# Optimization experiments

Measured on AMD Instinct MI355X. Metric: run time of the kernel, lower is better.

The kernel has to match this reference:

```python
import jax, jax.numpy as jnp
import numpy as np

T, B, D, H = 512, 64, 256, 512


def setup_inputs() -> dict:
    key = jax.random.key(0)
    ks = jax.random.split(key, 6)
    scale = 1.0 / np.sqrt(D + H)
    return {
        "seqs": jax.random.normal(ks[0], (T, B, D), dtype=jnp.float32),
        "h": jnp.zeros((B, H), dtype=jnp.float32),
        "C": jnp.zeros((B, H), dtype=jnp.float32),
        "Wi": jax.random.normal(ks[1], (H, D + H), dtype=jnp.float32) * scale,
        "bi": jnp.zeros((H,), dtype=jnp.float32),
        "Wf": jax.random.normal(ks[2], (H, D + H), dtype=jnp.float32) * scale,
        "bf": jnp.zeros((H,), dtype=jnp.float32),
        "Wg": jax.random.normal(ks[3], (H, D + H), dtype=jnp.float32) * scale,
        "bg": jnp.zeros((H,), dtype=jnp.float32),
        "Wo": jax.random.normal(ks[4], (H, D + H), dtype=jnp.float32) * scale,
        "bo": jnp.zeros((H,), dtype=jnp.float32),
    }


def reference(seqs, h, C, Wi, bi, Wf, bf, Wg, bg, Wo, bo):
    # Fuse the 4 gate Linears into one matmul: W [4H, D+H], b [4H].
    W = jnp.concatenate([Wi, Wf, Wg, Wo], axis=0)
    b = jnp.concatenate([bi, bf, bg, bo], axis=0)

    def step(carry, x):
        h_t, c_t = carry
        merge = jnp.concatenate([h_t, x], axis=1)  # [B, H+D] (h first, as in torch code)
        gates = merge @ W.T + b                    # [B, 4H]
        i, f, g, o = jnp.split(gates, 4, axis=1)
        c_new = jax.nn.sigmoid(f) * c_t + jax.nn.sigmoid(i) * jnp.tanh(g)
        h_new = jax.nn.sigmoid(o) * jnp.tanh(c_new)
        return (h_new, c_new), h_new

    (_, cT), hs = jax.lax.scan(step, (h, C), seqs)
    allhidden = jnp.concatenate([h[None], hs], axis=0)  # [T+1, B, H], includes initial h
    return allhidden, cT
```

## Files before the change

### kernel.cpp

```cpp
#include <hip/hip_runtime.h>


#define TSTEPS 512
#define BATCH 64
#define DIN 256
#define HID 512
#define KTOT 768
#define BHID (BATCH * HID)
#define NB 8
#define NU 16
#define VROW 1064
#define POISON 0x7f7f7f7fu

typedef __attribute__((ext_vector_type(8))) short bf16x8;
typedef __attribute__((ext_vector_type(4))) float f32x4;

__device__ __forceinline__ float4 llc_load4(const float* p) {
    float4 r; asm volatile("global_load_dwordx4 %0, %1, off sc0 sc1" : "=v"(r) : "v"(p)); return r;
}
__device__ __forceinline__ float llc_load1(const float* p) {
    float r; asm volatile("global_load_dword %0, %1, off sc0 sc1" : "=v"(r) : "v"(p)); return r;
}
__device__ __forceinline__ void llc_store1(float* p, float v) {
    asm volatile("global_store_dword %0, %1, off sc0 sc1" :: "v"(p), "v"(v) : "memory");
}
__device__ __forceinline__ unsigned short f2bf(float f) {
    unsigned u = __float_as_uint(f);
    return (unsigned short)((u + 0x7fffu + ((u >> 16) & 1u)) >> 16);
}

__global__ __launch_bounds__(256, 1)
void lstm_persistent(const float* __restrict__ seqs,
                     const float* __restrict__ h0,
                     const float* __restrict__ c0,
                     const float* __restrict__ Wi, const float* __restrict__ bi,
                     const float* __restrict__ Wf, const float* __restrict__ bff,
                     const float* __restrict__ Wg, const float* __restrict__ bg,
                     const float* __restrict__ Wo, const float* __restrict__ bo,
                     float* __restrict__ out)
{
    __shared__ __align__(16) short vv[NB * VROW];
    __shared__ float red[4][16][12];
    __shared__ float c_s[128];
    __shared__ float bias_s[64];

    const int tid  = threadIdx.x;
    const int bid  = blockIdx.x;
    const int g    = bid >> 5;
    const int rblk = bid & 31;
    const int b0 = g * NB;
    const int u0 = rblk * NU;

    const int w   = tid >> 6;
    const int l   = tid & 63;
    const int n16 = l & 15;
    const int khi = (l >> 4) & 3;
    const int bbr = l & 7;

    const float* Wsel = (w == 0) ? Wi : (w == 1) ? Wf : (w == 2) ? Wg : Wo;
    const float* wrow = Wsel + (size_t)(u0 + n16) * KTOT;
    bf16x8 whi[24], wlo[24];
#pragma unroll
    for (int kt = 0; kt < 24; ++kt) {
        const int k0 = kt * 32 + khi * 8;
        const float4 a = *reinterpret_cast<const float4*>(wrow + k0);
        const float4 b = *reinterpret_cast<const float4*>(wrow + k0 + 4);
        const float vals[8] = {a.x, a.y, a.z, a.w, b.x, b.y, b.z, b.w};
        bf16x8 h8, l8;
#pragma unroll
        for (int i = 0; i < 8; ++i) {
            const unsigned short hv = f2bf(vals[i]);
            h8[i] = (short)hv;
            l8[i] = (short)f2bf(vals[i] - __uint_as_float((unsigned)hv << 16));
        }
        whi[kt] = h8; wlo[kt] = l8;
    }

    if (tid < 64) {
        const int gg = tid >> 4, uu = tid & 15;
        const float* bsel = (gg == 0) ? bi : (gg == 1) ? bff : (gg == 2) ? bg : bo;
        bias_s[tid] = bsel[u0 + uu];
    }
    if (tid < 128) {
        const int uu = tid & 15, bb = tid >> 4;
        c_s[tid] = c0[(size_t)(b0 + bb) * HID + u0 + uu];
        out[(size_t)(b0 + bb) * HID + u0 + uu] = h0[(size_t)(b0 + bb) * HID + u0 + uu];
    }

    {
        const int b = tid >> 5, k0 = (tid & 31) * 16;
        const float* hp = h0 + (size_t)(b0 + b) * HID + k0;
        float hv[16];
#pragma unroll
        for (int i = 0; i < 4; ++i) {
            const float4 t4 = reinterpret_cast<const float4*>(hp)[i];
            hv[4*i] = t4.x; hv[4*i+1] = t4.y; hv[4*i+2] = t4.z; hv[4*i+3] = t4.w;
        }
        bf16x8 a8, b8;
#pragma unroll
        for (int i = 0; i < 8; ++i) { a8[i] = (short)f2bf(hv[i]); b8[i] = (short)f2bf(hv[8+i]); }
        *reinterpret_cast<bf16x8*>(&vv[b * VROW + k0])     = a8;
        *reinterpret_cast<bf16x8*>(&vv[b * VROW + k0 + 8]) = b8;
    }
    if (tid < 128) {
        const int b = tid >> 4, kx = (tid & 15) * 16;
        const float* xp = seqs + (size_t)(b0 + b) * DIN + kx;
        float xv[16];
#pragma unroll
        for (int i = 0; i < 4; ++i) {
            const float4 t4 = reinterpret_cast<const float4*>(xp)[i];
            xv[4*i] = t4.x; xv[4*i+1] = t4.y; xv[4*i+2] = t4.z; xv[4*i+3] = t4.w;
        }
        bf16x8 a8, b8, la8, lb8;
#pragma unroll
        for (int i = 0; i < 8; ++i) {
            const unsigned short h1 = f2bf(xv[i]);
            a8[i] = (short)h1; la8[i] = (short)f2bf(xv[i] - __uint_as_float((unsigned)h1 << 16));
            const unsigned short h2 = f2bf(xv[8+i]);
            b8[i] = (short)h2; lb8[i] = (short)f2bf(xv[8+i] - __uint_as_float((unsigned)h2 << 16));
        }
        *reinterpret_cast<bf16x8*>(&vv[b * VROW + 512 + kx])     = a8;
        *reinterpret_cast<bf16x8*>(&vv[b * VROW + 512 + kx + 8]) = b8;
        *reinterpret_cast<bf16x8*>(&vv[b * VROW + 768 + kx])     = la8;
        *reinterpret_cast<bf16x8*>(&vv[b * VROW + 768 + kx + 8]) = lb8;
    }
    __syncthreads();

    const short* vrow = &vv[bbr * VROW + khi * 8];

    for (int t = 0; t < TSTEPS; ++t) {
        f32x4 aA = {0.f,0.f,0.f,0.f}, aB = {0.f,0.f,0.f,0.f}, aC = {0.f,0.f,0.f,0.f};
#pragma unroll
        for (int kt = 0; kt < 8; ++kt) {
            const bf16x8 bh = *reinterpret_cast<const bf16x8*>(vrow + 512 + kt * 32);
            const bf16x8 bl = *reinterpret_cast<const bf16x8*>(vrow + 768 + kt * 32);
            aA = __builtin_amdgcn_mfma_f32_16x16x32_bf16(whi[16 + kt], bh, aA, 0, 0, 0);
            aB = __builtin_amdgcn_mfma_f32_16x16x32_bf16(wlo[16 + kt], bh, aB, 0, 0, 0);
            aC = __builtin_amdgcn_mfma_f32_16x16x32_bf16(whi[16 + kt], bl, aC, 0, 0, 0);
        }

        float4 xr[4];
        const bool do_x = (t + 1 < TSTEPS) && (tid < 128);
        if (do_x) {
            const float* xp = seqs + (size_t)(t + 1) * BATCH * DIN
                            + (size_t)(b0 + (tid >> 4)) * DIN + (tid & 15) * 16;
#pragma unroll
            for (int i = 0; i < 4; ++i) xr[i] = reinterpret_cast<const float4*>(xp)[i];
        }

        if (t > 0) {
            const float* srow = out + (size_t)t * BHID + (size_t)(b0 + 7) * HID;
            unsigned miss = 0;
            for (;;) {
                bool ok = true;
                if (l < 32) {
                    const float s = llc_load1(srow + l * 16 + 15);
                    asm volatile("s_waitcnt vmcnt(0)" ::: "memory");
                    __builtin_amdgcn_sched_barrier(0);
                    ok = (__float_as_uint(s) != POISON);
                }
                if (__all(ok)) break;
                if (++miss > (1u << 20)) break;
                __builtin_amdgcn_s_sleep(1);
            }
            const int b = tid >> 5, k0 = (tid & 31) * 16;
            const float* hp = out + (size_t)t * BHID + (size_t)(b0 + b) * HID + k0;
            float4 hb[4];
#pragma unroll
            for (int i = 0; i < 4; ++i) hb[i] = llc_load4(hp + 4 * i);
            asm volatile("s_waitcnt vmcnt(0)" ::: "memory");
            __builtin_amdgcn_sched_barrier(0);
            float hv[16];
#pragma unroll
            for (int i = 0; i < 4; ++i) {
                hv[4*i] = hb[i].x; hv[4*i+1] = hb[i].y; hv[4*i+2] = hb[i].z; hv[4*i+3] = hb[i].w;
            }
            bf16x8 a8, b8;
#pragma unroll
            for (int i = 0; i < 8; ++i) { a8[i] = (short)f2bf(hv[i]); b8[i] = (short)f2bf(hv[8+i]); }
            *reinterpret_cast<bf16x8*>(&vv[b * VROW + k0])     = a8;
            *reinterpret_cast<bf16x8*>(&vv[b * VROW + k0 + 8]) = b8;
        }
        __syncthreads();

#pragma unroll
        for (int kt = 0; kt < 16; ++kt) {
            const bf16x8 bh = *reinterpret_cast<const bf16x8*>(vrow + kt * 32);
            aA = __builtin_amdgcn_mfma_f32_16x16x32_bf16(whi[kt], bh, aA, 0, 0, 0);
            aB = __builtin_amdgcn_mfma_f32_16x16x32_bf16(wlo[kt], bh, aB, 0, 0, 0);
        }
        const f32x4 gAcc = aA + aB + aC;
        if (n16 < 8) {
#pragma unroll
            for (int r = 0; r < 4; ++r)
                red[w][khi * 4 + r][n16] = gAcc[r];
        }
        __syncthreads();

        float hn127 = 0.f;
        float* op127 = nullptr;
        if (tid < 128) {
            const int uu = tid & 15, bb = tid >> 4;
            const float gi = red[0][uu][bb] + bias_s[uu];
            const float gf = red[1][uu][bb] + bias_s[16 + uu];
            const float gG = red[2][uu][bb] + bias_s[32 + uu];
            const float go = red[3][uu][bb] + bias_s[48 + uu];
            const float i_ = 1.f / (1.f + __expf(-gi));
            const float f_ = 1.f / (1.f + __expf(-gf));
            const float o_ = 1.f / (1.f + __expf(-go));
            float eg = __expf(-2.f * fabsf(gG));
            float tg = (1.f - eg) / (1.f + eg);
            tg = (gG < 0.f) ? -tg : tg;
            const float cn = f_ * c_s[tid] + i_ * tg;
            c_s[tid] = cn;
            float ec = __expf(-2.f * fabsf(cn));
            float tc = (1.f - ec) / (1.f + ec);
            tc = (cn < 0.f) ? -tc : tc;
            const float hn = o_ * tc;
            float* op = out + (size_t)(t + 1) * BHID + (size_t)(b0 + bb) * HID + u0 + uu;
            if (tid != 127) llc_store1(op, hn);
            else { hn127 = hn; op127 = op; }
            if (t == TSTEPS - 1)
                out[(size_t)(TSTEPS + 1) * BHID + (size_t)(b0 + bb) * HID + u0 + uu] = cn;
        }

        if (do_x) {
            const int b = tid >> 4, kx = (tid & 15) * 16;
            float xv[16];
#pragma unroll
            for (int i = 0; i < 4; ++i) {
                xv[4*i] = xr[i].x; xv[4*i+1] = xr[i].y; xv[4*i+2] = xr[i].z; xv[4*i+3] = xr[i].w;
            }
            bf16x8 a8, b8, la8, lb8;
#pragma unroll
            for (int i = 0; i < 8; ++i) {
                const unsigned short h1 = f2bf(xv[i]);
                a8[i] = (short)h1; la8[i] = (short)f2bf(xv[i] - __uint_as_float((unsigned)h1 << 16));
                const unsigned short h2 = f2bf(xv[8+i]);
                b8[i] = (short)h2; lb8[i] = (short)f2bf(xv[8+i] - __uint_as_float((unsigned)h2 << 16));
            }
            *reinterpret_cast<bf16x8*>(&vv[b * VROW + 512 + kx])     = a8;
            *reinterpret_cast<bf16x8*>(&vv[b * VROW + 512 + kx + 8]) = b8;
            *reinterpret_cast<bf16x8*>(&vv[b * VROW + 768 + kx])     = la8;
            *reinterpret_cast<bf16x8*>(&vv[b * VROW + 768 + kx + 8]) = lb8;
        }

        asm volatile("s_waitcnt vmcnt(0)" ::: "memory");
        __syncthreads();
        if (tid == 127) llc_store1(op127, hn127);
    }
}

extern "C" void kernel_launch(void* const* d_in, const int* in_sizes, int n_in,
                              void* d_out, int out_size, void* d_ws, size_t ws_size,
                              hipStream_t stream) {
    const float* seqs = (const float*)d_in[0];
    const float* h0   = (const float*)d_in[1];
    const float* c0   = (const float*)d_in[2];
    const float* Wi   = (const float*)d_in[3];
    const float* bi   = (const float*)d_in[4];
    const float* Wf   = (const float*)d_in[5];
    const float* bf   = (const float*)d_in[6];
    const float* Wg   = (const float*)d_in[7];
    const float* bg   = (const float*)d_in[8];
    const float* Wo   = (const float*)d_in[9];
    const float* bo   = (const float*)d_in[10];
    float* out = (float*)d_out;

    hipMemsetAsync((char*)out + (size_t)BHID * 4, 0x7f,
                   (size_t)TSTEPS * BHID * 4, stream);

    hipLaunchKernelGGL(lstm_persistent, dim3(256), dim3(256), 0, stream,
                       seqs, h0, c0, Wi, bi, Wf, bf, Wg, bg, Wo, bo, out);
}
```

Baseline: 1.488 ms.

## Interleave gate rows per wave so each lane owns all four gates, poll data directly

Reorders the weight rows loaded into each wave so that the four gates of a unit land in one lane's MFMA accumulator. Each lane can then apply the LSTM cell update in registers, with the cell state and biases held in registers, which removes the shared-memory reduction and one block barrier per step. The cross-block handshake now polls the actual hidden-state loads until none are poison, instead of checking a flag element and then reloading. This drops the ordered last-store trick and the trailing vmcnt wait. The risk is that per-element polling relies on each value being stored atomically, and that spinning without sleep adds memory traffic.

After: 1.364 ms. 1.09x faster.

```diff
diff --git a/kernel.cpp b/kernel.cpp
--- a/kernel.cpp
+++ b/kernel.cpp
@@ -17,9 +17,6 @@
 
 __device__ __forceinline__ float4 llc_load4(const float* p) {
     float4 r; asm volatile("global_load_dwordx4 %0, %1, off sc0 sc1" : "=v"(r) : "v"(p)); return r;
-}
-__device__ __forceinline__ float llc_load1(const float* p) {
-    float r; asm volatile("global_load_dword %0, %1, off sc0 sc1" : "=v"(r) : "v"(p)); return r;
 }
 __device__ __forceinline__ void llc_store1(float* p, float v) {
     asm volatile("global_store_dword %0, %1, off sc0 sc1" :: "v"(p), "v"(v) : "memory");
@@ -40,9 +37,6 @@
                      float* __restrict__ out)
 {
     __shared__ __align__(16) short vv[NB * VROW];
-    __shared__ float red[4][16][12];
-    __shared__ float c_s[128];
-    __shared__ float bias_s[64];
 
     const int tid  = threadIdx.x;
     const int bid  = blockIdx.x;
@@ -51,14 +45,15 @@
     const int b0 = g * NB;
     const int u0 = rblk * NU;
 
-    const int w   = tid >> 6;
+    const int wv  = tid >> 6;
     const int l   = tid & 63;
     const int n16 = l & 15;
     const int khi = (l >> 4) & 3;
     const int bbr = l & 7;
 
-    const float* Wsel = (w == 0) ? Wi : (w == 1) ? Wf : (w == 2) ? Wg : Wo;
-    const float* wrow = Wsel + (size_t)(u0 + n16) * KTOT;
+    const int gsel = n16 & 3;
+    const float* Wsel = (gsel == 0) ? Wi : (gsel == 1) ? Wf : (gsel == 2) ? Wg : Wo;
+    const float* wrow = Wsel + (size_t)(u0 + 4 * wv + (n16 >> 2)) * KTOT;
     bf16x8 whi[24], wlo[24];
 #pragma unroll
     for (int kt = 0; kt < 24; ++kt) {
@@ -76,14 +71,14 @@
         whi[kt] = h8; wlo[kt] = l8;
     }
 
-    if (tid < 64) {
-        const int gg = tid >> 4, uu = tid & 15;
-        const float* bsel = (gg == 0) ? bi : (gg == 1) ? bff : (gg == 2) ? bg : bo;
-        bias_s[tid] = bsel[u0 + uu];
-    }
+    const int unit_d  = u0 + 4 * wv + khi;
+    const int batch_d = b0 + (n16 & 7);
+    const float bI = bi[unit_d],  bF = bff[unit_d];
+    const float bG = bg[unit_d],  bO = bo[unit_d];
+    float creg = c0[(size_t)batch_d * HID + unit_d];
+
     if (tid < 128) {
         const int uu = tid & 15, bb = tid >> 4;
-        c_s[tid] = c0[(size_t)(b0 + bb) * HID + u0 + uu];
         out[(size_t)(b0 + bb) * HID + u0 + uu] = h0[(size_t)(b0 + bb) * HID + u0 + uu];
     }
 
@@ -149,27 +144,26 @@
         }
 
         if (t > 0) {
-            const float* srow = out + (size_t)t * BHID + (size_t)(b0 + 7) * HID;
-            unsigned miss = 0;
-            for (;;) {
-                bool ok = true;
-                if (l < 32) {
-                    const float s = llc_load1(srow + l * 16 + 15);
-                    asm volatile("s_waitcnt vmcnt(0)" ::: "memory");
-                    __builtin_amdgcn_sched_barrier(0);
-                    ok = (__float_as_uint(s) != POISON);
-                }
-                if (__all(ok)) break;
-                if (++miss > (1u << 20)) break;
-                __builtin_amdgcn_s_sleep(1);
-            }
             const int b = tid >> 5, k0 = (tid & 31) * 16;
             const float* hp = out + (size_t)t * BHID + (size_t)(b0 + b) * HID + k0;
             float4 hb[4];
-#pragma unroll
-            for (int i = 0; i < 4; ++i) hb[i] = llc_load4(hp + 4 * i);
-            asm volatile("s_waitcnt vmcnt(0)" ::: "memory");
-            __builtin_amdgcn_sched_barrier(0);
+            unsigned miss = 0;
+            for (;;) {
+#pragma unroll
+                for (int i = 0; i < 4; ++i) hb[i] = llc_load4(hp + 4 * i);
+                asm volatile("s_waitcnt vmcnt(0)" ::: "memory");
+                __builtin_amdgcn_sched_barrier(0);
+                bool ok = true;
+#pragma unroll
+                for (int i = 0; i < 4; ++i) {
+                    ok &= (__float_as_uint(hb[i].x) != POISON);
+                    ok &= (__float_as_uint(hb[i].y) != POISON);
+                    ok &= (__float_as_uint(hb[i].z) != POISON);
+                    ok &= (__float_as_uint(hb[i].w) != POISON);
+                }
+                if (ok) break;
+                if (++miss > (1u << 20)) break;
+            }
             float hv[16];
 #pragma unroll
             for (int i = 0; i < 4; ++i) {
@@ -189,39 +183,27 @@
             aA = __builtin_amdgcn_mfma_f32_16x16x32_bf16(whi[kt], bh, aA, 0, 0, 0);
             aB = __builtin_amdgcn_mfma_f32_16x16x32_bf16(wlo[kt], bh, aB, 0, 0, 0);
         }
-        const f32x4 gAcc = aA + aB + aC;
+        const f32x4 gA = aA + aB + aC;
+
         if (n16 < 8) {
-#pragma unroll
-            for (int r = 0; r < 4; ++r)
-                red[w][khi * 4 + r][n16] = gAcc[r];
-        }
-        __syncthreads();
-
-        float hn127 = 0.f;
-        float* op127 = nullptr;
-        if (tid < 128) {
-            const int uu = tid & 15, bb = tid >> 4;
-            const float gi = red[0][uu][bb] + bias_s[uu];
-            const float gf = red[1][uu][bb] + bias_s[16 + uu];
-            const float gG = red[2][uu][bb] + bias_s[32 + uu];
-            const float go = red[3][uu][bb] + bias_s[48 + uu];
+            const float gi = gA[0] + bI;
+            const float gf = gA[1] + bF;
+            const float gG = gA[2] + bG;
+            const float go = gA[3] + bO;
             const float i_ = 1.f / (1.f + __expf(-gi));
             const float f_ = 1.f / (1.f + __expf(-gf));
             const float o_ = 1.f / (1.f + __expf(-go));
             float eg = __expf(-2.f * fabsf(gG));
             float tg = (1.f - eg) / (1.f + eg);
             tg = (gG < 0.f) ? -tg : tg;
-            const float cn = f_ * c_s[tid] + i_ * tg;
-            c_s[tid] = cn;
-            float ec = __expf(-2.f * fabsf(cn));
+            creg = f_ * creg + i_ * tg;
+            float ec = __expf(-2.f * fabsf(creg));
             float tc = (1.f - ec) / (1.f + ec);
-            tc = (cn < 0.f) ? -tc : tc;
+            tc = (creg < 0.f) ? -tc : tc;
             const float hn = o_ * tc;
-            float* op = out + (size_t)(t + 1) * BHID + (size_t)(b0 + bb) * HID + u0 + uu;
-            if (tid != 127) llc_store1(op, hn);
-            else { hn127 = hn; op127 = op; }
+            llc_store1(out + (size_t)(t + 1) * BHID + (size_t)batch_d * HID + unit_d, hn);
             if (t == TSTEPS - 1)
-                out[(size_t)(TSTEPS + 1) * BHID + (size_t)(b0 + bb) * HID + u0 + uu] = cn;
+                out[(size_t)(TSTEPS + 1) * BHID + (size_t)batch_d * HID + unit_d] = creg;
         }
 
         if (do_x) {
@@ -244,10 +226,7 @@
             *reinterpret_cast<bf16x8*>(&vv[b * VROW + 768 + kx])     = la8;
             *reinterpret_cast<bf16x8*>(&vv[b * VROW + 768 + kx + 8]) = lb8;
         }
-
-        asm volatile("s_waitcnt vmcnt(0)" ::: "memory");
         __syncthreads();
-        if (tid == 127) llc_store1(op127, hn127);
     }
 }
 
```
